# Performance work log

Hardware: AMD Instinct MI355X
Metric: run time of the kernel (lower is better)

The kernel has to match this reference:

```python
import jax, jax.numpy as jnp
import numpy as np

# Dims: B=2, S=2048, D=1024 hidden, E=8 experts, F=2752 ffn (SwiGLU), top-1 gate,
# capacity_factor=1.0 -> capacity C = (B*S)//E = 512. Residual-MoE (moe_use_residual=True).

def setup_inputs() -> dict:
    key = jax.random.key(0)
    ks = jax.random.split(key, 10)
    B, S, D, E, F = 2, 2048, 1024, 8, 2752
    sc = 0.02
    return {
        "hidden_states": jax.random.normal(ks[0], (B, S, D), jnp.float32),
        "wg":  jax.random.normal(ks[1], (D, E), jnp.float32) * sc,   # gate
        "w1":  jax.random.normal(ks[2], (E, D, F), jnp.float32) * sc,  # expert SwiGLU
        "w3":  jax.random.normal(ks[3], (E, D, F), jnp.float32) * sc,
        "w2":  jax.random.normal(ks[4], (E, F, D), jnp.float32) * sc,
        "rw1": jax.random.normal(ks[5], (D, F), jnp.float32) * sc,    # residual MLP (SwiGLU, no bias)
        "rw3": jax.random.normal(ks[6], (D, F), jnp.float32) * sc,
        "rw2": jax.random.normal(ks[7], (F, D), jnp.float32) * sc,
        "cw":  jax.random.normal(ks[8], (D, 2), jnp.float32) * sc,    # coefficient Linear(D, 2)
        "cb":  jnp.zeros((2,), jnp.float32),
    }


def _moe_forward(x, wg, w1, w3, w2):
    """GShard/DeepSpeed-style top-1 gated MoE with capacity + token dropping.
    x: [T, D] flattened tokens. Returns (out [T,D], l_aux scalar, exp_counts [E])."""
    T, D = x.shape
    E = wg.shape[1]
    C = max(4, T // E)  # capacity_factor = 1.0, min_capacity = 4

    logits = x @ wg                                  # [T, E]
    gates = jax.nn.softmax(logits, axis=-1)
    idx = jnp.argmax(gates, axis=-1)                 # top-1 expert per token
    mask1 = jax.nn.one_hot(idx, E, dtype=gates.dtype)  # [T, E]
    exp_counts = jnp.sum(mask1, axis=0).astype(jnp.int32)

    # load-balancing aux loss (DeepSpeed top1gating)
    me = jnp.mean(gates, axis=0)
    ce = jnp.mean(mask1, axis=0)
    l_aux = jnp.sum(me * ce) * E

    # position of each token within its expert's buffer; drop overflow
    locations = jnp.cumsum(mask1, axis=0) - 1.0      # [T, E]
    mask1 = mask1 * (locations < C)
    loc_s = jnp.sum(locations * mask1, axis=1).astype(jnp.int32)  # [T]
    gates1 = jnp.sum(gates * mask1, axis=1)          # [T] gate weight (0 if dropped)

    loc_oh = jax.nn.one_hot(loc_s, C, dtype=gates.dtype)          # [T, C]
    combine = gates1[:, None, None] * mask1[:, :, None] * loc_oh[:, None, :]  # [T, E, C]
    dispatch = (combine > 0).astype(x.dtype)

    xe = jnp.einsum("tec,td->ecd", dispatch, x)      # dispatch to [E, C, D]
    h = jax.nn.silu(jnp.einsum("ecd,edf->ecf", xe, w1)) * jnp.einsum("ecd,edf->ecf", xe, w3)
    ye = jnp.einsum("ecf,efd->ecd", h, w2)           # expert SwiGLU FFN
    out = jnp.einsum("tec,ecd->td", combine, ye)     # weighted combine back to tokens
    return out, l_aux, exp_counts


def reference(hidden_states, wg, w1, w3, w2, rw1, rw3, rw2, cw, cb):
    B, S, D = hidden_states.shape
    x = hidden_states.reshape(-1, D)
    moe_out, l_aux, exp_counts = _moe_forward(x, wg, w1, w3, w2)
    moe_out = moe_out.reshape(B, S, D)

    # residual SwiGLU MLP + softmax-gated combine (Residual-MoE)
    mlp = (jax.nn.silu(hidden_states @ rw1) * (hidden_states @ rw3)) @ rw2
    coef = jax.nn.softmax(hidden_states @ cw + cb, axis=-1)  # [B, S, 2]
    output = moe_out * coef[..., 0:1] + mlp * coef[..., 1:2]
    return output, l_aux, exp_counts
```

## Files before the change

### kernel.cpp

```cpp
#include <hip/hip_runtime.h>
#include <hip/hip_bf16.h>
#include <stdint.h>

#define T_TOK 4096
#define DD 1024
#define EE 8
#define CC 512
#define FF 2752

typedef __attribute__((ext_vector_type(8))) short bf16x8;
typedef __attribute__((ext_vector_type(4))) float f32x4;
typedef __attribute__((ext_vector_type(4))) unsigned short us4;
typedef __attribute__((ext_vector_type(8))) unsigned short us8;

__device__ __forceinline__ float bf2f(unsigned short u) {
  union { float f; unsigned int i; } v; v.i = ((unsigned int)u) << 16; return v.f;
}
__device__ __forceinline__ unsigned short f2bf(float f) {
  union { float f; unsigned int i; } v; v.f = f;
  unsigned int r = v.i + 0x7fffu + ((v.i >> 16) & 1u);
  return (unsigned short)(r >> 16);
}

#define GLDS16(g, l) __builtin_amdgcn_global_load_lds( \
    (const __attribute__((address_space(1))) void*)(g), \
    (__attribute__((address_space(3))) void*)(l), 16, 0, 0)

#define STG_CHUNK(l) (((l & 3) ^ ((l >> 3) & 3)) * 8)
#define RD_OFF(fr, fq) ((fr) * 32 + (((fq) ^ (((fr) >> 1) & 3)) * 8))

#define BAR() do { asm volatile("" ::: "memory"); __builtin_amdgcn_s_barrier(); \
                   asm volatile("" ::: "memory"); } while (0)

__global__ __launch_bounds__(256)
void transpose_k(const float* __restrict__ in, const float* __restrict__ in2,
                 unsigned short* __restrict__ out, unsigned short* __restrict__ out2,
                 int R, int C, long inStride, long outStride) {
  __shared__ float smf[64][65];
  int b = blockIdx.z;
  if (b < EE) { in += (long)b * inStride; out += (long)b * outStride; }
  else { in = in2; out = out2; }
  int cb = blockIdx.x * 64, rb = blockIdx.y * 64;
  int t = threadIdx.x;
  int rr = t >> 4, c4 = (t & 15) * 4;
#pragma unroll
  for (int i = 0; i < 4; ++i) {
    int r = rr + i * 16;
    float4 v = *(const float4*)(in + (long)(rb + r) * C + cb + c4);
    smf[c4 + 0][r] = v.x;
    smf[c4 + 1][r] = v.y;
    smf[c4 + 2][r] = v.z;
    smf[c4 + 3][r] = v.w;
  }
  __syncthreads();
#pragma unroll
  for (int j = 0; j < 2; ++j) {
    int idx = t + j * 256;
    int g = idx & 7, c = idx >> 3;
    int r8 = g * 8;
    us8 o;
#pragma unroll
    for (int k = 0; k < 8; ++k) o[k] = f2bf(smf[c][r8 + k]);
    *(us8*)(out + (long)(cb + c) * R + rb + r8) = o;
  }
}

__global__ void zero_me_k(float* me) { if (threadIdx.x < EE) me[threadIdx.x] = 0.0f; }

__global__ void gate_k(const float* __restrict__ x, const float* __restrict__ wg,
                       const float* __restrict__ cw, const float* __restrict__ cbv,
                       int* __restrict__ idx, float* __restrict__ gatev,
                       float* __restrict__ coef, float* __restrict__ me_sum) {
  int tid = threadIdx.x, lane = tid & 63, wv = tid >> 6;
  int t = blockIdx.x * 4 + wv;
  const float* xr = x + (long)t * DD;
  float acc[EE] = {0,0,0,0,0,0,0,0};
  float c0 = 0.0f, c1 = 0.0f;
  for (int d = lane; d < DD; d += 64) {
    float xv = xr[d];
#pragma unroll
    for (int e = 0; e < EE; ++e) acc[e] += xv * wg[d * EE + e];
    c0 += xv * cw[d * 2 + 0];
    c1 += xv * cw[d * 2 + 1];
  }
#pragma unroll
  for (int o = 32; o > 0; o >>= 1) {
#pragma unroll
    for (int e = 0; e < EE; ++e) acc[e] += __shfl_xor(acc[e], o);
    c0 += __shfl_xor(c0, o);
    c1 += __shfl_xor(c1, o);
  }
  __shared__ float sme[EE];
  if (tid < EE) sme[tid] = 0.0f;
  __syncthreads();
  if (lane == 0) {
    float m = acc[0]; int am = 0;
#pragma unroll
    for (int e = 1; e < EE; ++e) if (acc[e] > m) { m = acc[e]; am = e; }
    float g[EE]; float s = 0.0f;
#pragma unroll
    for (int e = 0; e < EE; ++e) { g[e] = __expf(acc[e] - m); s += g[e]; }
    float inv = 1.0f / s;
    idx[t] = am;
    gatev[t] = g[am] * inv;
#pragma unroll
    for (int e = 0; e < EE; ++e) atomicAdd(&sme[e], g[e] * inv);
    float l0 = c0 + cbv[0], l1 = c1 + cbv[1];
    float mm = fmaxf(l0, l1);
    float e0 = __expf(l0 - mm), e1 = __expf(l1 - mm);
    float is = 1.0f / (e0 + e1);
    coef[t * 2 + 0] = e0 * is;
    coef[t * 2 + 1] = e1 * is;
  }
  __syncthreads();
  if (tid < EE) atomicAdd(&me_sum[tid], sme[tid]);
}

__global__ void scan_k(const int* __restrict__ idx, const float* __restrict__ me_sum,
                       int* __restrict__ slot, int* __restrict__ tok,
                       float* __restrict__ out_tail) {
  __shared__ int sidx[T_TOK];
  __shared__ int counts[EE];
  int tid = threadIdx.x;
  for (int i = tid; i < T_TOK; i += 512) sidx[i] = idx[i];
  __syncthreads();
  int e = tid >> 6, lane = tid & 63;
  int base = 0;
  for (int it = 0; it < T_TOK / 64; ++it) {
    int t = it * 64 + lane;
    bool f = (sidx[t] == e);
    unsigned long long m = __ballot(f);
    if (f) {
      int loc = base + __popcll(m & ((1ull << lane) - 1ull));
      slot[t] = (loc < CC) ? loc : -1;
      if (loc < CC) tok[e * CC + loc] = t;
    }
    base += __popcll(m);
  }
  if (lane == 0) counts[e] = base;
  __syncthreads();
  int filled = min(counts[e], CC);
  for (int c = filled + lane; c < CC; c += 64) tok[e * CC + c] = -1;
  if (tid == 0) {
    float la = 0.0f;
    for (int i = 0; i < EE; ++i) la += me_sum[i] * (float)counts[i];
    la *= (float)EE / ((float)T_TOK * (float)T_TOK);
    out_tail[0] = la;
    for (int i = 0; i < EE; ++i) out_tail[1 + i] = (float)counts[i];
  }
}

__global__ void gather_k(const float* __restrict__ x, const int* __restrict__ tok,
                         unsigned short* __restrict__ xb, unsigned short* __restrict__ xe) {
  int r = blockIdx.x, tid = threadIdx.x;
  int d = tid * 4;
  if (r < T_TOK) {
    float4 v = *(const float4*)(x + (long)r * DD + d);
    us4 o; o.x = f2bf(v.x); o.y = f2bf(v.y); o.z = f2bf(v.z); o.w = f2bf(v.w);
    *(us4*)(xb + (long)r * DD + d) = o;
  } else {
    int s = r - T_TOK;
    int t = tok[s];
    us4 o = {0, 0, 0, 0};
    if (t >= 0) {
      float4 v = *(const float4*)(x + (long)t * DD + d);
      o.x = f2bf(v.x); o.y = f2bf(v.y); o.z = f2bf(v.z); o.w = f2bf(v.w);
    }
    *(us4*)(xe + (long)s * DD + d) = o;
  }
}

__global__ __launch_bounds__(512, 2)
void gemm1_k(const unsigned short* __restrict__ xcat,
             const float* __restrict__ w1, const float* __restrict__ w3,
             const float* __restrict__ rw1, const float* __restrict__ rw3,
             unsigned short* __restrict__ Hcat) {
  int lin = blockIdx.x;
  int work = (lin & 7) * 88 + (lin >> 3);
  int mtile, ntile;
  if (work < 352) {
    int e = work / 44, r = work - e * 44;
    ntile = r >> 1;
    mtile = e * 2 + (r & 1);
  } else {
    int q = work - 352;
    ntile = q >> 4;
    mtile = 16 + (q & 15);
  }
  const unsigned short* A = xcat + (size_t)mtile * 256 * DD;
  const float *B1, *B3;
  if (mtile < 16) { int e = mtile >> 1; B1 = w1 + (size_t)e * DD * FF; B3 = w3 + (size_t)e * DD * FF; }
  else { B1 = rw1; B3 = rw3; }
  unsigned short* H = Hcat + (size_t)mtile * 256 * FF;
  int n0 = ntile * 128;

  __shared__ __align__(16) char Lc[147456];
  const unsigned short* ldsS = (const unsigned short*)Lc;

  int tid = threadIdx.x, l = tid & 63, w = tid >> 6;
  int wm = w >> 2, wn = w & 3;
  int fr = l & 15, fq = l >> 4;
  int srow = l >> 2, soff = STG_CHUNK(l);
  int rdo = RD_OFF(fr, fq);

  const unsigned short* gA0 = A + (size_t)(w * 16 + srow) * DD + soff;
  const unsigned short* gA1 = A + (size_t)((8 + w) * 16 + srow) * DD + soff;
  int lrow = l >> 5;
  int kl0 = 2 * w + lrow;
  int kl1 = 16 + 2 * w + lrow;
  int cs0 = (l & 31) ^ (((kl0 >> 3) & 1) << 2);
  int cs1 = (l & 31) ^ (((kl1 >> 3) & 1) << 2);
  int nn0 = n0 + 4 * cs0; if (nn0 >= FF) nn0 = 0;
  int nn1 = n0 + 4 * cs1; if (nn1 >= FF) nn1 = 0;
  const float* gB1a = B1 + (size_t)kl0 * FF + nn0;
  const float* gB1b = B1 + (size_t)kl1 * FF + nn1;
  const float* gB3a = B3 + (size_t)kl0 * FF + nn0;
  const float* gB3b = B3 + (size_t)kl1 * FF + nn1;

  int cb[2];
#pragma unroll
  for (int ni = 0; ni < 2; ++ni)
    cb[ni] = fq * 4096 + ((((wn * 2 + ni) * 64 + fr * 4)) ^ ((fq & 1) << 6));

#define STG1(bb, hw) do { size_t ka = (size_t)(hw) * 32; size_t kb = ka * FF;   \
    GLDS16(gA0 + ka, Lc + (bb) * 16384 + w * 1024);                             \
    GLDS16(gA1 + ka, Lc + (bb) * 16384 + (8 + w) * 1024);                       \
    GLDS16(gB1a + kb, Lc + 49152 + (bb) * 16384 + w * 1024);                    \
    GLDS16(gB1b + kb, Lc + 49152 + (bb) * 16384 + (8 + w) * 1024);              \
    GLDS16(gB3a + kb, Lc + 98304 + (bb) * 16384 + w * 1024);                    \
    GLDS16(gB3b + kb, Lc + 98304 + (bb) * 16384 + (8 + w) * 1024); } while (0)

  f32x4 acc1[8][2] = {};
  f32x4 acc3[8][2] = {};

  const int HN = 32;
  STG1(0, 0);
  STG1(1, 1);

  for (int h = 0; h < HN; ++h) {
    int buf = h % 3;
    int hw = h + 2; if (hw >= HN) hw -= HN;
    int bufw = (buf + 2) % 3;

    asm volatile("s_waitcnt vmcnt(6)" ::: "memory");
    BAR();
    STG1(bufw, hw);

    const char* Bb1 = Lc + 49152 + buf * 16384;
    const char* Bb3 = Lc + 98304 + buf * 16384;
    bf16x8 af[8];
#pragma unroll
    for (int mi = 0; mi < 8; ++mi)
      af[mi] = *(const bf16x8*)(ldsS + buf * 8192 + (wm * 8 + mi) * 512 + rdo);

    {
      float fb[2][8];
#pragma unroll
      for (int ni = 0; ni < 2; ++ni)
#pragma unroll
        for (int j = 0; j < 8; ++j)
          fb[ni][j] = *(const float*)(Bb1 + cb[ni] + j * 512);
      __builtin_amdgcn_s_setprio(1);
#pragma unroll
      for (int ni = 0; ni < 2; ++ni) {
        union { bf16x8 h; unsigned int u[4]; } bu;
#pragma unroll
        for (int p = 0; p < 4; ++p)
          asm("v_cvt_pk_bf16_f32 %0, %1, %2" : "=v"(bu.u[p]) : "v"(fb[ni][2 * p]), "v"(fb[ni][2 * p + 1]));
#pragma unroll
        for (int mi = 0; mi < 8; ++mi)
          acc1[mi][ni] = __builtin_amdgcn_mfma_f32_16x16x32_bf16(af[mi], bu.h, acc1[mi][ni], 0, 0, 0);
      }
      __builtin_amdgcn_s_setprio(0);
    }
    {
      float fb[2][8];
#pragma unroll
      for (int ni = 0; ni < 2; ++ni)
#pragma unroll
        for (int j = 0; j < 8; ++j)
          fb[ni][j] = *(const float*)(Bb3 + cb[ni] + j * 512);
      __builtin_amdgcn_s_setprio(1);
#pragma unroll
      for (int ni = 0; ni < 2; ++ni) {
        union { bf16x8 h; unsigned int u[4]; } bu;
#pragma unroll
        for (int p = 0; p < 4; ++p)
          asm("v_cvt_pk_bf16_f32 %0, %1, %2" : "=v"(bu.u[p]) : "v"(fb[ni][2 * p]), "v"(fb[ni][2 * p + 1]));
#pragma unroll
        for (int mi = 0; mi < 8; ++mi)
          acc3[mi][ni] = __builtin_amdgcn_mfma_f32_16x16x32_bf16(af[mi], bu.h, acc3[mi][ni], 0, 0, 0);
      }
      __builtin_amdgcn_s_setprio(0);
    }
  }
#undef STG1

#pragma unroll
  for (int mi = 0; mi < 8; ++mi)
#pragma unroll
    for (int ni = 0; ni < 2; ++ni)
#pragma unroll
      for (int r = 0; r < 4; ++r) {
        int gm = wm * 128 + mi * 16 + fq * 4 + r;
        int gn = n0 + (wn * 2 + ni) * 16 + fr;
        if (gn < FF) {
          float v1 = acc1[mi][ni][r], v3 = acc3[mi][ni][r];
          float h = v1 / (1.0f + __expf(-v1)) * v3;
          H[(size_t)gm * FF + gn] = f2bf(h);
        }
      }
}

__global__ __launch_bounds__(512, 2)
void gemm2_k(const unsigned short* __restrict__ Hcat,
             const unsigned short* __restrict__ w2t, const unsigned short* __restrict__ rw2t,
             unsigned short* __restrict__ Ycat) {
  int lin = blockIdx.x;
  int work = (lin & 7) * 32 + (lin >> 3);
  int mtile, ntile;
  if (work < 128) {
    int e = work >> 4, r = work & 15;
    ntile = r >> 1;
    mtile = e * 2 + (r & 1);
  } else {
    int q = work - 128;
    ntile = q >> 4;
    mtile = 16 + (q & 15);
  }
  const unsigned short* A = Hcat + (size_t)mtile * 256 * FF;
  const unsigned short* B = (mtile < 16) ? (w2t + (size_t)(mtile >> 1) * (size_t)DD * FF) : rw2t;
  unsigned short* Y = Ycat + (size_t)mtile * 256 * DD;
  int n0 = ntile * 128;

  __shared__ __align__(16) unsigned short lds[73728];
  char* Lc = (char*)lds;

  int tid = threadIdx.x, l = tid & 63, w = tid >> 6;
  int wm = w >> 1, wn = w & 1;
  int fr = l & 15, fq = l >> 4;
  int srow = l >> 2, soff = STG_CHUNK(l);
  int rdo = RD_OFF(fr, fq);

  const unsigned short* gA0 = A + (size_t)(w * 16 + srow) * FF + soff;
  const unsigned short* gA1 = A + (size_t)((8 + w) * 16 + srow) * FF + soff;
  const unsigned short* gB  = B + (size_t)(n0 + w * 16 + srow) * FF + soff;

#define STG2(bb, kk) do {                                          \
    GLDS16(gA0 + (kk), Lc + (bb) * 16384 + w * 1024);              \
    GLDS16(gA1 + (kk), Lc + (bb) * 16384 + (8 + w) * 1024);        \
    GLDS16(gB  + (kk), Lc + 98304 + (bb) * 8192 + w * 1024); } while (0)

  f32x4 acc[4][4] = {};

  const int HN = 86;
#pragma unroll
  for (int hh = 0; hh < 5; ++hh) STG2(hh, hh * 32);
  asm volatile("s_waitcnt vmcnt(12)" ::: "memory");
  BAR();

  int b = 0;
#pragma unroll 2
  for (int h = 0; h < HN; ++h) {
    int bn = b ? b - 1 : 5;
    int hw = h + 5; if (hw >= HN) hw -= HN;
    int kk = hw * 32;
    bf16x8 af[4], bf[4];

#pragma unroll
    for (int mi = 0; mi < 4; ++mi)
      af[mi] = *(const bf16x8*)(lds + b * 8192 + (wm * 4 + mi) * 512 + rdo);
#pragma unroll
    for (int ni = 0; ni < 4; ++ni)
      bf[ni] = *(const bf16x8*)(lds + 49152 + b * 4096 + (wn * 4 + ni) * 512 + rdo);
    STG2(bn, kk);
    asm volatile("s_waitcnt vmcnt(12)" ::: "memory");
    BAR();
    __builtin_amdgcn_s_setprio(1);
#pragma unroll
    for (int mi = 0; mi < 4; ++mi)
#pragma unroll
      for (int ni = 0; ni < 4; ++ni)
        acc[mi][ni] = __builtin_amdgcn_mfma_f32_16x16x32_bf16(af[mi], bf[ni], acc[mi][ni], 0, 0, 0);
    __builtin_amdgcn_s_setprio(0);
    BAR();

    ++b; if (b == 6) b = 0;
  }
#undef STG2

#pragma unroll
  for (int mi = 0; mi < 4; ++mi)
#pragma unroll
    for (int ni = 0; ni < 4; ++ni)
#pragma unroll
      for (int r = 0; r < 4; ++r) {
        int gm = wm * 64 + mi * 16 + fq * 4 + r;
        int gn = n0 + wn * 64 + ni * 16 + fr;
        Y[(size_t)gm * DD + gn] = f2bf(acc[mi][ni][r]);
      }
}

__global__ void combine_k(const unsigned short* __restrict__ Ye, const unsigned short* __restrict__ Yr,
                          const int* __restrict__ idx, const int* __restrict__ slot,
                          const float* __restrict__ gatev, const float* __restrict__ coef,
                          float* __restrict__ out) {
  int t = blockIdx.x, tid = threadIdx.x;
  int d = tid * 4;
  float c0 = coef[t * 2], c1 = coef[t * 2 + 1];
  int s = slot[t];
  float g = gatev[t] * c0;
  us4 vr = *(const us4*)(Yr + (size_t)t * DD + d);
  float4 o;
  if (s >= 0) {
    us4 ve = *(const us4*)(Ye + ((size_t)idx[t] * CC + s) * DD + d);
    o.x = g * bf2f(ve.x) + c1 * bf2f(vr.x);
    o.y = g * bf2f(ve.y) + c1 * bf2f(vr.y);
    o.z = g * bf2f(ve.z) + c1 * bf2f(vr.z);
    o.w = g * bf2f(ve.w) + c1 * bf2f(vr.w);
  } else {
    o.x = c1 * bf2f(vr.x);
    o.y = c1 * bf2f(vr.y);
    o.z = c1 * bf2f(vr.z);
    o.w = c1 * bf2f(vr.w);
  }
  *(float4*)(out + (size_t)t * DD + d) = o;
}

extern "C" void kernel_launch(void* const* d_in, const int* in_sizes, int n_in,
                              void* d_out, int out_size, void* d_ws, size_t ws_size,
                              hipStream_t stream) {
  const float* x   = (const float*)d_in[0];
  const float* wg  = (const float*)d_in[1];
  const float* w1  = (const float*)d_in[2];
  const float* w3  = (const float*)d_in[3];
  const float* w2  = (const float*)d_in[4];
  const float* rw1 = (const float*)d_in[5];
  const float* rw3 = (const float*)d_in[6];
  const float* rw2 = (const float*)d_in[7];
  const float* cw  = (const float*)d_in[8];
  const float* cbv = (const float*)d_in[9];
  float* out = (float*)d_out;

  char* ws = (char*)d_ws;
  size_t o = 0;
  auto alloc = [&](size_t bytes) -> char* {
    char* p = ws + o; o = (o + bytes + 255) & ~(size_t)255; return p;
  };
  unsigned short* w2t  = (unsigned short*)alloc((size_t)EE * DD * FF * 2);
  unsigned short* rw2t = (unsigned short*)alloc((size_t)DD * FF * 2);
  unsigned short* xe   = (unsigned short*)alloc((size_t)T_TOK * DD * 2);
  unsigned short* xb   = (unsigned short*)alloc((size_t)T_TOK * DD * 2);
  unsigned short* He   = (unsigned short*)alloc((size_t)T_TOK * FF * 2);
  unsigned short* Hr   = (unsigned short*)alloc((size_t)T_TOK * FF * 2);
  unsigned short* Ye   = (unsigned short*)alloc((size_t)T_TOK * DD * 2);
  unsigned short* Yr   = (unsigned short*)alloc((size_t)T_TOK * DD * 2);
  int*   idxp  = (int*)alloc(T_TOK * 4);
  float* gatev = (float*)alloc(T_TOK * 4);
  int*   slotp = (int*)alloc(T_TOK * 4);
  int*   tokp  = (int*)alloc(EE * CC * 4);
  float* coefp = (float*)alloc(T_TOK * 2 * 4);
  float* mep   = (float*)alloc(256);
  if (o > ws_size) return;

  transpose_k<<<dim3(16, 43, EE + 1), 256, 0, stream>>>(w2, rw2, w2t, rw2t, FF, DD, (long)FF * DD, (long)DD * FF);

  zero_me_k<<<1, 64, 0, stream>>>(mep);
  gate_k<<<T_TOK / 4, 256, 0, stream>>>(x, wg, cw, cbv, idxp, gatev, coefp, mep);
  scan_k<<<1, 512, 0, stream>>>(idxp, mep, slotp, tokp, out + (size_t)T_TOK * DD);
  gather_k<<<2 * T_TOK, 256, 0, stream>>>(x, tokp, xb, xe);
  gemm1_k<<<704, 512, 0, stream>>>(xe, w1, w3, rw1, rw3, He);
  gemm2_k<<<256, 512, 0, stream>>>(He, w2t, rw2t, Ye);
  combine_k<<<T_TOK, 256, 0, stream>>>(Ye, Yr, idxp, slotp, gatev, coefp, out);
}
```

Baseline: 266.7 us.

## Shrink gemm1 tiles and load fp32 weights straight to registers instead of LDS

```diff
diff --git a/kernel.cpp b/kernel.cpp
--- a/kernel.cpp
+++ b/kernel.cpp
@@ -170,145 +170,129 @@
   }
 }
 
-__global__ __launch_bounds__(512, 2)
+__global__ __launch_bounds__(256, 3)
 void gemm1_k(const unsigned short* __restrict__ xcat,
              const float* __restrict__ w1, const float* __restrict__ w3,
              const float* __restrict__ rw1, const float* __restrict__ rw3,
              unsigned short* __restrict__ Hcat) {
   int lin = blockIdx.x;
-  int work = (lin & 7) * 88 + (lin >> 3);
+  int work = (lin & 7) * 344 + (lin >> 3);
   int mtile, ntile;
-  if (work < 352) {
-    int e = work / 44, r = work - e * 44;
-    ntile = r >> 1;
-    mtile = e * 2 + (r & 1);
+  if (work < 1376) {
+    int e = work / 172, r = work - e * 172;
+    ntile = r >> 2;
+    mtile = e * 4 + (r & 3);
   } else {
-    int q = work - 352;
-    ntile = q >> 4;
-    mtile = 16 + (q & 15);
-  }
-  const unsigned short* A = xcat + (size_t)mtile * 256 * DD;
+    int q = work - 1376;
+    ntile = q >> 5;
+    mtile = 32 + (q & 31);
+  }
+  const unsigned short* A = xcat + (size_t)mtile * 128 * DD;
   const float *B1, *B3;
-  if (mtile < 16) { int e = mtile >> 1; B1 = w1 + (size_t)e * DD * FF; B3 = w3 + (size_t)e * DD * FF; }
+  if (mtile < 32) { int e = mtile >> 2; B1 = w1 + (size_t)e * DD * FF; B3 = w3 + (size_t)e * DD * FF; }
   else { B1 = rw1; B3 = rw3; }
-  unsigned short* H = Hcat + (size_t)mtile * 256 * FF;
-  int n0 = ntile * 128;
-
-  __shared__ __align__(16) char Lc[147456];
+  unsigned short* H = Hcat + (size_t)mtile * 128 * FF;
+  int n0 = ntile * 64;
+
+  __shared__ __align__(16) char Lc[32768];
   const unsigned short* ldsS = (const unsigned short*)Lc;
 
   int tid = threadIdx.x, l = tid & 63, w = tid >> 6;
-  int wm = w >> 2, wn = w & 3;
+  int wm = w >> 1, wn = w & 1;
   int fr = l & 15, fq = l >> 4;
   int srow = l >> 2, soff = STG_CHUNK(l);
   int rdo = RD_OFF(fr, fq);
 
   const unsigned short* gA0 = A + (size_t)(w * 16 + srow) * DD + soff;
-  const unsigned short* gA1 = A + (size_t)((8 + w) * 16 + srow) * DD + soff;
-  int lrow = l >> 5;
-  int kl0 = 2 * w + lrow;
-  int kl1 = 16 + 2 * w + lrow;
-  int cs0 = (l & 31) ^ (((kl0 >> 3) & 1) << 2);
-  int cs1 = (l & 31) ^ (((kl1 >> 3) & 1) << 2);
-  int nn0 = n0 + 4 * cs0; if (nn0 >= FF) nn0 = 0;
-  int nn1 = n0 + 4 * cs1; if (nn1 >= FF) nn1 = 0;
-  const float* gB1a = B1 + (size_t)kl0 * FF + nn0;
-  const float* gB1b = B1 + (size_t)kl1 * FF + nn1;
-  const float* gB3a = B3 + (size_t)kl0 * FF + nn0;
-  const float* gB3b = B3 + (size_t)kl1 * FF + nn1;
-
-  int cb[2];
-#pragma unroll
-  for (int ni = 0; ni < 2; ++ni)
-    cb[ni] = fq * 4096 + ((((wn * 2 + ni) * 64 + fr * 4)) ^ ((fq & 1) << 6));
-
-#define STG1(bb, hw) do { size_t ka = (size_t)(hw) * 32; size_t kb = ka * FF;   \
-    GLDS16(gA0 + ka, Lc + (bb) * 16384 + w * 1024);                             \
-    GLDS16(gA1 + ka, Lc + (bb) * 16384 + (8 + w) * 1024);                       \
-    GLDS16(gB1a + kb, Lc + 49152 + (bb) * 16384 + w * 1024);                    \
-    GLDS16(gB1b + kb, Lc + 49152 + (bb) * 16384 + (8 + w) * 1024);              \
-    GLDS16(gB3a + kb, Lc + 98304 + (bb) * 16384 + w * 1024);                    \
-    GLDS16(gB3b + kb, Lc + 98304 + (bb) * 16384 + (8 + w) * 1024); } while (0)
-
-  f32x4 acc1[8][2] = {};
-  f32x4 acc3[8][2] = {};
+  const unsigned short* gA1 = A + (size_t)((4 + w) * 16 + srow) * DD + soff;
+
+  int ncol = n0 + wn * 32 + fr;
+  int ofs0[8];
+#pragma unroll
+  for (int j = 0; j < 8; ++j) ofs0[j] = (fq * 8 + j) * FF + ncol;
+
+#define STGA(bb, hh) do { size_t ka = (size_t)(hh) * 32;                      \
+    GLDS16(gA0 + ka, Lc + (bb) * 8192 + w * 1024);                            \
+    GLDS16(gA1 + ka, Lc + (bb) * 8192 + (4 + w) * 1024); } while (0)
+
+  float R0[2][8], R1[2][8];
+  auto bload1 = [&](int kb) {
+    const float* p = B1 + kb;
+#pragma unroll
+    for (int j = 0; j < 8; ++j) { R0[0][j] = p[ofs0[j]]; R0[1][j] = p[ofs0[j] + 16]; }
+  };
+  auto bload3 = [&](int kb) {
+    const float* p = B3 + kb;
+#pragma unroll
+    for (int j = 0; j < 8; ++j) { R1[0][j] = p[ofs0[j]]; R1[1][j] = p[ofs0[j] + 16]; }
+  };
+
+  f32x4 acc1[4][2] = {};
+  f32x4 acc3[4][2] = {};
 
   const int HN = 32;
-  STG1(0, 0);
-  STG1(1, 1);
+  STGA(0, 0); STGA(1, 1); STGA(2, 2);
+  bload1(0);
+  bload3(0);
 
   for (int h = 0; h < HN; ++h) {
-    int buf = h % 3;
-    int hw = h + 2; if (hw >= HN) hw -= HN;
-    int bufw = (buf + 2) % 3;
-
-    asm volatile("s_waitcnt vmcnt(6)" ::: "memory");
+    int ab = h & 3, sb = (h + 3) & 3;
+    int hw3 = h + 3; if (hw3 >= HN) hw3 -= HN;
+    int hw1 = h + 1; if (hw1 >= HN) hw1 -= HN;
+    int kb1 = hw1 * 32 * FF;
+
+    asm volatile("s_waitcnt vmcnt(16)" ::: "memory");
     BAR();
-    STG1(bufw, hw);
-
-    const char* Bb1 = Lc + 49152 + buf * 16384;
-    const char* Bb3 = Lc + 98304 + buf * 16384;
-    bf16x8 af[8];
-#pragma unroll
-    for (int mi = 0; mi < 8; ++mi)
-      af[mi] = *(const bf16x8*)(ldsS + buf * 8192 + (wm * 8 + mi) * 512 + rdo);
-
-    {
-      float fb[2][8];
-#pragma unroll
-      for (int ni = 0; ni < 2; ++ni)
-#pragma unroll
-        for (int j = 0; j < 8; ++j)
-          fb[ni][j] = *(const float*)(Bb1 + cb[ni] + j * 512);
-      __builtin_amdgcn_s_setprio(1);
-#pragma unroll
-      for (int ni = 0; ni < 2; ++ni) {
-        union { bf16x8 h; unsigned int u[4]; } bu;
-#pragma unroll
-        for (int p = 0; p < 4; ++p)
-          asm("v_cvt_pk_bf16_f32 %0, %1, %2" : "=v"(bu.u[p]) : "v"(fb[ni][2 * p]), "v"(fb[ni][2 * p + 1]));
-#pragma unroll
-        for (int mi = 0; mi < 8; ++mi)
-          acc1[mi][ni] = __builtin_amdgcn_mfma_f32_16x16x32_bf16(af[mi], bu.h, acc1[mi][ni], 0, 0, 0);
-      }
-      __builtin_amdgcn_s_setprio(0);
+    STGA(sb, hw3);
+
+    bf16x8 af[4];
+#pragma unroll
+    for (int mi = 0; mi < 4; ++mi)
+      af[mi] = *(const bf16x8*)(ldsS + ab * 4096 + (wm * 4 + mi) * 512 + rdo);
+
+    __builtin_amdgcn_s_setprio(1);
+#pragma unroll
+    for (int ni = 0; ni < 2; ++ni) {
+      union { bf16x8 hh; unsigned int u[4]; } bu;
+#pragma unroll
+      for (int p = 0; p < 4; ++p)
+        asm("v_cvt_pk_bf16_f32 %0, %1, %2" : "=v"(bu.u[p]) : "v"(R0[ni][2 * p]), "v"(R0[ni][2 * p + 1]));
+#pragma unroll
+      for (int mi = 0; mi < 4; ++mi)
+        acc1[mi][ni] = __builtin_amdgcn_mfma_f32_16x16x32_bf16(af[mi], bu.hh, acc1[mi][ni], 0, 0, 0);
     }
-    {
-      float fb[2][8];
-#pragma unroll
-      for (int ni = 0; ni < 2; ++ni)
-#pragma unroll
-        for (int j = 0; j < 8; ++j)
-          fb[ni][j] = *(const float*)(Bb3 + cb[ni] + j * 512);
-      __builtin_amdgcn_s_setprio(1);
-#pragma unroll
-      for (int ni = 0; ni < 2; ++ni) {
-        union { bf16x8 h; unsigned int u[4]; } bu;
-#pragma unroll
-        for (int p = 0; p < 4; ++p)
-          asm("v_cvt_pk_bf16_f32 %0, %1, %2" : "=v"(bu.u[p]) : "v"(fb[ni][2 * p]), "v"(fb[ni][2 * p + 1]));
-#pragma unroll
-        for (int mi = 0; mi < 8; ++mi)
-          acc3[mi][ni] = __builtin_amdgcn_mfma_f32_16x16x32_bf16(af[mi], bu.h, acc3[mi][ni], 0, 0, 0);
-      }
-      __builtin_amdgcn_s_setprio(0);
+    __builtin_amdgcn_s_setprio(0);
+    bload1(kb1);
+
+    asm volatile("s_waitcnt vmcnt(18)" ::: "memory");
+
+    __builtin_amdgcn_s_setprio(1);
+#pragma unroll
+    for (int ni = 0; ni < 2; ++ni) {
+      union { bf16x8 hh; unsigned int u[4]; } bu;
+#pragma unroll
+      for (int p = 0; p < 4; ++p)
+        asm("v_cvt_pk_bf16_f32 %0, %1, %2" : "=v"(bu.u[p]) : "v"(R1[ni][2 * p]), "v"(R1[ni][2 * p + 1]));
+#pragma unroll
+      for (int mi = 0; mi < 4; ++mi)
+        acc3[mi][ni] = __builtin_amdgcn_mfma_f32_16x16x32_bf16(af[mi], bu.hh, acc3[mi][ni], 0, 0, 0);
     }
-  }
-#undef STG1
-
-#pragma unroll
-  for (int mi = 0; mi < 8; ++mi)
+    __builtin_amdgcn_s_setprio(0);
+    bload3(kb1);
+  }
+#undef STGA
+
+#pragma unroll
+  for (int mi = 0; mi < 4; ++mi)
 #pragma unroll
     for (int ni = 0; ni < 2; ++ni)
 #pragma unroll
       for (int r = 0; r < 4; ++r) {
-        int gm = wm * 128 + mi * 16 + fq * 4 + r;
-        int gn = n0 + (wn * 2 + ni) * 16 + fr;
-        if (gn < FF) {
-          float v1 = acc1[mi][ni][r], v3 = acc3[mi][ni][r];
-          float h = v1 / (1.0f + __expf(-v1)) * v3;
-          H[(size_t)gm * FF + gn] = f2bf(h);
-        }
+        int gm = wm * 64 + mi * 16 + fq * 4 + r;
+        int gn = n0 + wn * 32 + ni * 16 + fr;
+        float v1 = acc1[mi][ni][r], v3 = acc3[mi][ni][r];
+        float hv = v1 / (1.0f + __expf(-v1)) * v3;
+        H[(size_t)gm * FF + gn] = f2bf(hv);
       }
 }
 
@@ -469,7 +453,7 @@
   gate_k<<<T_TOK / 4, 256, 0, stream>>>(x, wg, cw, cbv, idxp, gatev, coefp, mep);
   scan_k<<<1, 512, 0, stream>>>(idxp, mep, slotp, tokp, out + (size_t)T_TOK * DD);
   gather_k<<<2 * T_TOK, 256, 0, stream>>>(x, tokp, xb, xe);
-  gemm1_k<<<704, 512, 0, stream>>>(xe, w1, w3, rw1, rw3, He);
+  gemm1_k<<<2752, 256, 0, stream>>>(xe, w1, w3, rw1, rw3, He);
   gemm2_k<<<256, 512, 0, stream>>>(He, w2t, rw2t, Ye);
   combine_k<<<T_TOK, 256, 0, stream>>>(Ye, Yr, idxp, slotp, gatev, coefp, out);
 }
```

After: 347.9 us. +30.4%, slower.
